# Kernel optimization log

Hardware: AMD Instinct MI355X
Metric: run time of the kernel (lower is better)

Reference implementation:

```python
import jax, jax.numpy as jnp
import numpy as np

B, T, F, H = 32, 8192, 256, 128


def setup_inputs() -> dict:
    key = jax.random.key(0)
    k1, k2, k3, k4, k5 = jax.random.split(key, 5)
    return {
        "encoder_outputs": jax.random.normal(k1, (B, T, F), dtype=jnp.float32),
        "dec_output": jax.random.normal(k2, (B, F), dtype=jnp.float32),
        "W1": jax.random.normal(k3, (F, H), dtype=jnp.float32) * 0.05,
        "W2": jax.random.normal(k4, (F, H), dtype=jnp.float32) * 0.05,
        "V": jax.random.normal(k5, (H, 1), dtype=jnp.float32) * 0.05,
    }


def reference(encoder_outputs, dec_output, W1, W2, V):
    # w1_e: [B,T,H]; w2_d: [B,1,H] (constant across timesteps, no real recurrence)
    w1_e = jnp.einsum("btf,fh->bth", encoder_outputs, W1)
    w2_d = (dec_output @ W2)[:, None, :]
    # scores[b,t] = V . tanh(W1 e_t + W2 d)  -> [B, T] (raw logits, no softmax in original call)
    scores = jnp.einsum("bth,h->bt", jnp.tanh(w1_e + w2_d), V[:, 0])
    return scores
```

## Files before the change

### kernel.cpp

```cpp
#include <hip/hip_runtime.h>

#define B_ 32
#define T_ 8192
#define F_ 256
#define H_ 128

typedef short bf16x8 __attribute__((ext_vector_type(8)));
typedef float f32x4  __attribute__((ext_vector_type(4)));

static __device__ __forceinline__ unsigned int pack_bf2(float lo, float hi) {
    unsigned int r;
    asm("v_cvt_pk_bf16_f32 %0, %1, %2" : "=v"(r) : "v"(lo), "v"(hi));
    return r;
}

static __device__ __forceinline__ float fast_tanh(float x) {
    float e = __builtin_amdgcn_exp2f(x * 2.8853900817779268f);
    return 1.f - 2.f * __builtin_amdgcn_rcpf(e + 1.f);
}

__global__ __launch_bounds__(512) void attn_fused(const float* __restrict__ enc,
                                                  const float* __restrict__ dec,
                                                  const float* __restrict__ W1,
                                                  const float* __restrict__ W2,
                                                  const float* __restrict__ Vvec,
                                                  float* __restrict__ out) {
    __shared__ __align__(16) unsigned char tile_lds[2][32 * 512];
    __shared__ float red[8][512];
    __shared__ float w2dp[4][128];
    __shared__ float w2dv[128];

    const int tid  = threadIdx.x;
    const int blk  = blockIdx.x;
    const int b    = blk >> 4;
    const int t0   = (blk & 15) << 9;
    const int w    = tid >> 6;
    const int lane = tid & 63;
    const int q    = lane >> 4;
    const int c    = lane & 15;

    const f32x4* src = (const f32x4*)(enc + ((size_t)b * T_ + t0) * F_);

    f32x4 x[4];
    #pragma unroll
    for (int i = 0; i < 4; ++i) x[i] = src[i * 512 + tid];

    const int h = 16 * w + c;
    bf16x8 bw[8];
    #pragma unroll
    for (int ks = 0; ks < 8; ++ks) {
        const float* wp = W1 + (64 * q + 8 * ks) * H_ + h;
        union { bf16x8 v; unsigned int u[4]; } pk;
        #pragma unroll
        for (int jj = 0; jj < 4; ++jj)
            pk.u[jj] = pack_bf2(wp[(2 * jj) * H_], wp[(2 * jj + 1) * H_]);
        bw[ks] = pk.v;
    }

    {
        const int hh = tid & 127, p = tid >> 7;
        const float* dp  = dec + b * F_ + p * 64;
        const float* w2p = W2 + (p * 64) * H_ + hh;
        float s = 0.f;
        #pragma unroll 8
        for (int f = 0; f < 64; ++f) s += dp[f] * w2p[f * H_];
        w2dp[p][hh] = s;
    }
    __syncthreads();
    if (tid < 128)
        w2dv[tid] = w2dp[0][tid] + w2dp[1][tid] + w2dp[2][tid] + w2dp[3][tid];
    __syncthreads();

    const float Vv = Vvec[h];
    const float wd = w2dv[h];
    const int sw = c & 7;

    #pragma unroll 2
    for (int ht = 0; ht < 16; ++ht) {
        unsigned char* buf = tile_lds[ht & 1];

        #pragma unroll
        for (int i = 0; i < 4; ++i) {
            const int flat4 = i * 512 + tid;
            const int row   = flat4 >> 6;
            const int c4    = flat4 & 63;
            const int chunk = (c4 >> 1) ^ (row & 7);
            uint2 v;
            v.x = pack_bf2(x[i][0], x[i][1]);
            v.y = pack_bf2(x[i][2], x[i][3]);
            *(uint2*)(buf + row * 512 + chunk * 16 + (c4 & 1) * 8) = v;
        }

        if (ht < 15) {
            const f32x4* sp = src + (ht + 1) * 2048;
            #pragma unroll
            for (int i = 0; i < 4; ++i) x[i] = sp[i * 512 + tid];
        }

        asm volatile("s_waitcnt lgkmcnt(0)\n\ts_barrier" ::: "memory");

        #pragma unroll
        for (int g = 0; g < 2; ++g) {
            const unsigned char* rbase = buf + (g * 16 + c) * 512;
            f32x4 acc = {0.f, 0.f, 0.f, 0.f};
            #pragma unroll
            for (int ks = 0; ks < 8; ++ks) {
                bf16x8 a = *(const bf16x8*)(rbase + ((8 * q + ks) ^ sw) * 16);
                acc = __builtin_amdgcn_mfma_f32_16x16x32_bf16(a, bw[ks], acc, 0, 0, 0);
            }
            f32x4 part;
            #pragma unroll
            for (int r = 0; r < 4; ++r)
                part[r] = Vv * fast_tanh(acc[r] + wd);
            #pragma unroll
            for (int m = 1; m < 16; m <<= 1) {
                #pragma unroll
                for (int r = 0; r < 4; ++r) part[r] += __shfl_xor(part[r], m, 64);
            }
            if (c == 0)
                *(f32x4*)&red[w][ht * 32 + g * 16 + 4 * q] = part;
        }
    }

    __syncthreads();
    float s = 0.f;
    #pragma unroll
    for (int ww = 0; ww < 8; ++ww) s += red[ww][tid];
    out[(size_t)b * T_ + t0 + tid] = s;
}

extern "C" void kernel_launch(void* const* d_in, const int* in_sizes, int n_in,
                              void* d_out, int out_size, void* d_ws, size_t ws_size,
                              hipStream_t stream) {
    const float* enc = (const float*)d_in[0];
    const float* dec = (const float*)d_in[1];
    const float* W1  = (const float*)d_in[2];
    const float* W2  = (const float*)d_in[3];
    const float* V   = (const float*)d_in[4];
    float* out = (float*)d_out;

    attn_fused<<<512, 512, 0, stream>>>(enc, dec, W1, W2, V, out);
}
```

Baseline: 53.85 us.

## Swap MFMA operands so the H dimension lands in rows and shrink blocks to 256 threads

The kernel now uses 256-thread blocks over 256 timesteps, with 1024 blocks in total. Each wave covers 32 hidden units as two 16-wide N tiles and shares one LDS read of the encoder tile between two MFMAs. The MFMA operands are swapped so W1 is the A operand, which puts hidden units across the accumulator rows. The V-weighted tanh sum can then be reduced inside each lane over 8 values, leaving only two cross-lane shuffles instead of sixteen. It also adds s_setprio around the MFMA loop and halves LDS usage per block, which allows more blocks per CU, at the cost of twice the bf16 W1 fragments held in registers.

Result: slower. 58.40 us (+8.5%).

```diff
diff --git a/kernel.cpp b/kernel.cpp
--- a/kernel.cpp
+++ b/kernel.cpp
@@ -19,22 +19,22 @@
     return 1.f - 2.f * __builtin_amdgcn_rcpf(e + 1.f);
 }
 
-__global__ __launch_bounds__(512) void attn_fused(const float* __restrict__ enc,
+__global__ __launch_bounds__(256) void attn_fused(const float* __restrict__ enc,
                                                   const float* __restrict__ dec,
                                                   const float* __restrict__ W1,
                                                   const float* __restrict__ W2,
                                                   const float* __restrict__ Vvec,
                                                   float* __restrict__ out) {
-    __shared__ __align__(16) unsigned char tile_lds[2][32 * 512];
-    __shared__ float red[8][512];
-    __shared__ float w2dp[4][128];
+    __shared__ __align__(16) unsigned char tile_lds[2][16 * 512];
+    __shared__ float red[4][256];
+    __shared__ float w2dp[2][128];
     __shared__ float w2dv[128];
 
     const int tid  = threadIdx.x;
     const int blk  = blockIdx.x;
-    const int b    = blk >> 4;
-    const int t0   = (blk & 15) << 9;
-    const int w    = tid >> 6;
+    const int b    = blk >> 5;
+    const int t0   = (blk & 31) << 8;
+    const int wh   = tid >> 6;
     const int lane = tid & 63;
     const int q    = lane >> 4;
     const int c    = lane & 15;
@@ -43,45 +43,53 @@
 
     f32x4 x[4];
     #pragma unroll
-    for (int i = 0; i < 4; ++i) x[i] = src[i * 512 + tid];
+    for (int i = 0; i < 4; ++i) x[i] = src[i * 256 + tid];
 
-    const int h = 16 * w + c;
-    bf16x8 bw[8];
+    bf16x8 bw[2][8];
     #pragma unroll
-    for (int ks = 0; ks < 8; ++ks) {
-        const float* wp = W1 + (64 * q + 8 * ks) * H_ + h;
-        union { bf16x8 v; unsigned int u[4]; } pk;
+    for (int ntl = 0; ntl < 2; ++ntl) {
+        const int h = 32 * wh + 16 * ntl + c;
         #pragma unroll
-        for (int jj = 0; jj < 4; ++jj)
-            pk.u[jj] = pack_bf2(wp[(2 * jj) * H_], wp[(2 * jj + 1) * H_]);
-        bw[ks] = pk.v;
+        for (int ks = 0; ks < 8; ++ks) {
+            const float* wp = W1 + (64 * q + 8 * ks) * H_ + h;
+            union { bf16x8 v; unsigned int u[4]; } pk;
+            #pragma unroll
+            for (int jj = 0; jj < 4; ++jj)
+                pk.u[jj] = pack_bf2(wp[(2 * jj) * H_], wp[(2 * jj + 1) * H_]);
+            bw[ntl][ks] = pk.v;
+        }
     }
 
     {
         const int hh = tid & 127, p = tid >> 7;
-        const float* dp  = dec + b * F_ + p * 64;
-        const float* w2p = W2 + (p * 64) * H_ + hh;
+        const float* dp  = dec + b * F_ + p * 128;
+        const float* w2p = W2 + (p * 128) * H_ + hh;
         float s = 0.f;
         #pragma unroll 8
-        for (int f = 0; f < 64; ++f) s += dp[f] * w2p[f * H_];
+        for (int f = 0; f < 128; ++f) s += dp[f] * w2p[f * H_];
         w2dp[p][hh] = s;
     }
     __syncthreads();
-    if (tid < 128)
-        w2dv[tid] = w2dp[0][tid] + w2dp[1][tid] + w2dp[2][tid] + w2dp[3][tid];
+    if (tid < 128) w2dv[tid] = w2dp[0][tid] + w2dp[1][tid];
     __syncthreads();
 
-    const float Vv = Vvec[h];
-    const float wd = w2dv[h];
+    float Vv[2][4], wd[2][4];
+    #pragma unroll
+    for (int ntl = 0; ntl < 2; ++ntl)
+        #pragma unroll
+        for (int r = 0; r < 4; ++r) {
+            const int hr = 32 * wh + 16 * ntl + 4 * q + r;
+            Vv[ntl][r] = Vvec[hr];
+            wd[ntl][r] = w2dv[hr];
+        }
     const int sw = c & 7;
 
-    #pragma unroll 2
-    for (int ht = 0; ht < 16; ++ht) {
-        unsigned char* buf = tile_lds[ht & 1];
+    for (int st = 0; st < 16; ++st) {
+        unsigned char* buf = tile_lds[st & 1];
 
         #pragma unroll
         for (int i = 0; i < 4; ++i) {
-            const int flat4 = i * 512 + tid;
+            const int flat4 = i * 256 + tid;
             const int row   = flat4 >> 6;
             const int c4    = flat4 & 63;
             const int chunk = (c4 >> 1) ^ (row & 7);
@@ -91,42 +99,44 @@
             *(uint2*)(buf + row * 512 + chunk * 16 + (c4 & 1) * 8) = v;
         }
 
-        if (ht < 15) {
-            const f32x4* sp = src + (ht + 1) * 2048;
+        if (st < 15) {
+            const f32x4* sp = src + (st + 1) * 1024;
             #pragma unroll
-            for (int i = 0; i < 4; ++i) x[i] = sp[i * 512 + tid];
+            for (int i = 0; i < 4; ++i) x[i] = sp[i * 256 + tid];
         }
 
         asm volatile("s_waitcnt lgkmcnt(0)\n\ts_barrier" ::: "memory");
 
+        __builtin_amdgcn_s_setprio(1);
+        const unsigned char* rbase = buf + c * 512;
+        f32x4 a0 = {0.f, 0.f, 0.f, 0.f};
+        f32x4 a1 = {0.f, 0.f, 0.f, 0.f};
         #pragma unroll
-        for (int g = 0; g < 2; ++g) {
-            const unsigned char* rbase = buf + (g * 16 + c) * 512;
-            f32x4 acc = {0.f, 0.f, 0.f, 0.f};
-            #pragma unroll
-            for (int ks = 0; ks < 8; ++ks) {
-                bf16x8 a = *(const bf16x8*)(rbase + ((8 * q + ks) ^ sw) * 16);
-                acc = __builtin_amdgcn_mfma_f32_16x16x32_bf16(a, bw[ks], acc, 0, 0, 0);
-            }
-            f32x4 part;
-            #pragma unroll
-            for (int r = 0; r < 4; ++r)
-                part[r] = Vv * fast_tanh(acc[r] + wd);
-            #pragma unroll
-            for (int m = 1; m < 16; m <<= 1) {
-                #pragma unroll
-                for (int r = 0; r < 4; ++r) part[r] += __shfl_xor(part[r], m, 64);
-            }
-            if (c == 0)
-                *(f32x4*)&red[w][ht * 32 + g * 16 + 4 * q] = part;
+        for (int ks = 0; ks < 8; ++ks) {
+            bf16x8 be = *(const bf16x8*)(rbase + ((8 * q + ks) ^ sw) * 16);
+            a0 = __builtin_amdgcn_mfma_f32_16x16x32_bf16(bw[0][ks], be, a0, 0, 0, 0);
+            a1 = __builtin_amdgcn_mfma_f32_16x16x32_bf16(bw[1][ks], be, a1, 0, 0, 0);
         }
+        __builtin_amdgcn_s_setprio(0);
+
+        float part = Vv[0][0] * fast_tanh(a0[0] + wd[0][0])
+                   + Vv[0][1] * fast_tanh(a0[1] + wd[0][1])
+                   + Vv[0][2] * fast_tanh(a0[2] + wd[0][2])
+                   + Vv[0][3] * fast_tanh(a0[3] + wd[0][3])
+                   + Vv[1][0] * fast_tanh(a1[0] + wd[1][0])
+                   + Vv[1][1] * fast_tanh(a1[1] + wd[1][1])
+                   + Vv[1][2] * fast_tanh(a1[2] + wd[1][2])
+                   + Vv[1][3] * fast_tanh(a1[3] + wd[1][3]);
+        part += __shfl_xor(part, 16, 64);
+        part += __shfl_xor(part, 32, 64);
+        if (lane < 16) red[wh][st * 16 + c] = part;
     }
 
     __syncthreads();
-    float s = 0.f;
-    #pragma unroll
-    for (int ww = 0; ww < 8; ++ww) s += red[ww][tid];
-    out[(size_t)b * T_ + t0 + tid] = s;
+    {
+        float s = red[0][tid] + red[1][tid] + red[2][tid] + red[3][tid];
+        out[(size_t)b * T_ + t0 + tid] = s;
+    }
 }
 
 extern "C" void kernel_launch(void* const* d_in, const int* in_sizes, int n_in,
@@ -139,5 +149,5 @@
     const float* V   = (const float*)d_in[4];
     float* out = (float*)d_out;
 
-    attn_fused<<<512, 512, 0, stream>>>(enc, dec, W1, W2, V, out);
+    attn_fused<<<1024, 256, 0, stream>>>(enc, dec, W1, W2, V, out);
 }
```

## Transpose MFMA operands so each wave covers 32 hidden units and 16 rows

Applied to the files above, without the earlier changes.

Remaps waves so each handles 32 hidden columns (two 16-wide N tiles) over one 16-row group, with W1 as the A operand and the encoder tile as B. This puts hidden units along accumulator rows, so the V-weighted tanh sum happens mostly within a lane and needs only two cross-lane shuffles instead of sixteen. The W2·d bias is folded in as the initial accumulator. Register use for W1 fragments doubles, the final reduction drops from 8 to 4 partial arrays, and the ht loop unroll pragma is removed.

New measurement: 55.19 us. +2.5%, slower.

```diff
diff --git a/kernel.cpp b/kernel.cpp
--- a/kernel.cpp
+++ b/kernel.cpp
@@ -26,7 +26,7 @@
                                                   const float* __restrict__ Vvec,
                                                   float* __restrict__ out) {
     __shared__ __align__(16) unsigned char tile_lds[2][32 * 512];
-    __shared__ float red[8][512];
+    __shared__ float red[4][512];
     __shared__ float w2dp[4][128];
     __shared__ float w2dv[128];
 
@@ -35,6 +35,8 @@
     const int b    = blk >> 4;
     const int t0   = (blk & 15) << 9;
     const int w    = tid >> 6;
+    const int wh   = w & 3;
+    const int wg   = w >> 2;
     const int lane = tid & 63;
     const int q    = lane >> 4;
     const int c    = lane & 15;
@@ -45,16 +47,19 @@
     #pragma unroll
     for (int i = 0; i < 4; ++i) x[i] = src[i * 512 + tid];
 
-    const int h = 16 * w + c;
-    bf16x8 bw[8];
+    bf16x8 bw[2][8];
     #pragma unroll
-    for (int ks = 0; ks < 8; ++ks) {
-        const float* wp = W1 + (64 * q + 8 * ks) * H_ + h;
-        union { bf16x8 v; unsigned int u[4]; } pk;
+    for (int ntl = 0; ntl < 2; ++ntl) {
+        const int h = 32 * wh + 16 * ntl + c;
         #pragma unroll
-        for (int jj = 0; jj < 4; ++jj)
-            pk.u[jj] = pack_bf2(wp[(2 * jj) * H_], wp[(2 * jj + 1) * H_]);
-        bw[ks] = pk.v;
+        for (int ks = 0; ks < 8; ++ks) {
+            const float* wp = W1 + (64 * q + 8 * ks) * H_ + h;
+            union { bf16x8 v; unsigned int u[4]; } pk;
+            #pragma unroll
+            for (int jj = 0; jj < 4; ++jj)
+                pk.u[jj] = pack_bf2(wp[(2 * jj) * H_], wp[(2 * jj + 1) * H_]);
+            bw[ntl][ks] = pk.v;
+        }
     }
 
     {
@@ -71,11 +76,18 @@
         w2dv[tid] = w2dp[0][tid] + w2dp[1][tid] + w2dp[2][tid] + w2dp[3][tid];
     __syncthreads();
 
-    const float Vv = Vvec[h];
-    const float wd = w2dv[h];
+    f32x4 wd0, wd1;
+    float Vv[2][4];
+    #pragma unroll
+    for (int r = 0; r < 4; ++r) {
+        const int h0 = 32 * wh + 4 * q + r;
+        wd0[r] = w2dv[h0];
+        wd1[r] = w2dv[h0 + 16];
+        Vv[0][r] = Vvec[h0];
+        Vv[1][r] = Vvec[h0 + 16];
+    }
     const int sw = c & 7;
 
-    #pragma unroll 2
     for (int ht = 0; ht < 16; ++ht) {
         unsigned char* buf = tile_lds[ht & 1];
 
@@ -99,34 +111,34 @@
 
         asm volatile("s_waitcnt lgkmcnt(0)\n\ts_barrier" ::: "memory");
 
+        const unsigned char* rbase = buf + (wg * 16 + c) * 512;
+        f32x4 a0 = wd0;
+        f32x4 a1 = wd1;
         #pragma unroll
-        for (int g = 0; g < 2; ++g) {
-            const unsigned char* rbase = buf + (g * 16 + c) * 512;
-            f32x4 acc = {0.f, 0.f, 0.f, 0.f};
-            #pragma unroll
-            for (int ks = 0; ks < 8; ++ks) {
-                bf16x8 a = *(const bf16x8*)(rbase + ((8 * q + ks) ^ sw) * 16);
-                acc = __builtin_amdgcn_mfma_f32_16x16x32_bf16(a, bw[ks], acc, 0, 0, 0);
-            }
-            f32x4 part;
-            #pragma unroll
-            for (int r = 0; r < 4; ++r)
-                part[r] = Vv * fast_tanh(acc[r] + wd);
-            #pragma unroll
-            for (int m = 1; m < 16; m <<= 1) {
-                #pragma unroll
-                for (int r = 0; r < 4; ++r) part[r] += __shfl_xor(part[r], m, 64);
-            }
-            if (c == 0)
-                *(f32x4*)&red[w][ht * 32 + g * 16 + 4 * q] = part;
+        for (int ks = 0; ks < 8; ++ks) {
+            bf16x8 be = *(const bf16x8*)(rbase + ((8 * q + ks) ^ sw) * 16);
+            a0 = __builtin_amdgcn_mfma_f32_16x16x32_bf16(bw[0][ks], be, a0, 0, 0, 0);
+            a1 = __builtin_amdgcn_mfma_f32_16x16x32_bf16(bw[1][ks], be, a1, 0, 0, 0);
         }
+
+        float part = Vv[0][0] * fast_tanh(a0[0])
+                   + Vv[0][1] * fast_tanh(a0[1])
+                   + Vv[0][2] * fast_tanh(a0[2])
+                   + Vv[0][3] * fast_tanh(a0[3])
+                   + Vv[1][0] * fast_tanh(a1[0])
+                   + Vv[1][1] * fast_tanh(a1[1])
+                   + Vv[1][2] * fast_tanh(a1[2])
+                   + Vv[1][3] * fast_tanh(a1[3]);
+        part += __shfl_xor(part, 16, 64);
+        part += __shfl_xor(part, 32, 64);
+        if (lane < 16) red[wh][ht * 32 + wg * 16 + c] = part;
     }
 
     __syncthreads();
-    float s = 0.f;
-    #pragma unroll
-    for (int ww = 0; ww < 8; ++ww) s += red[ww][tid];
-    out[(size_t)b * T_ + t0 + tid] = s;
+    {
+        float s = red[0][tid] + red[1][tid] + red[2][tid] + red[3][tid];
+        out[(size_t)b * T_ + t0 + tid] = s;
+    }
 }
 
 extern "C" void kernel_launch(void* const* d_in, const int* in_sizes, int n_in,
```

## Swap MFMA operands, double tile depth, and pipeline per-tile score reduction

Applied to the files above, without the earlier changes.

The MFMA operands are swapped so each lane's four accumulator values cover four hidden units of one timestep. The V-weighted tanh sum then folds within each lane, and only two cross-lane shuffles are needed instead of sixteen. The tile per iteration grows from 32 to 64 timesteps, with 8 prefetched float4 loads per thread, so there are half as many barrier-separated steps. The final cross-wave reduction moves into the loop behind a double-buffered reduction array. This costs more registers and twice the LDS for the tile, which may lower occupancy.

Result: faster. 52.00 us (-3.4%).

```diff
diff --git a/kernel.cpp b/kernel.cpp
--- a/kernel.cpp
+++ b/kernel.cpp
@@ -25,8 +25,8 @@
                                                   const float* __restrict__ W2,
                                                   const float* __restrict__ Vvec,
                                                   float* __restrict__ out) {
-    __shared__ __align__(16) unsigned char tile_lds[2][32 * 512];
-    __shared__ float red[8][512];
+    __shared__ __align__(16) unsigned char tile_lds[2][64 * 512];
+    __shared__ float red[2][8][64];
     __shared__ float w2dp[4][128];
     __shared__ float w2dv[128];
 
@@ -41,9 +41,9 @@
 
     const f32x4* src = (const f32x4*)(enc + ((size_t)b * T_ + t0) * F_);
 
-    f32x4 x[4];
+    f32x4 x[8];
     #pragma unroll
-    for (int i = 0; i < 4; ++i) x[i] = src[i * 512 + tid];
+    for (int i = 0; i < 8; ++i) x[i] = src[i * 512 + tid];
 
     const int h = 16 * w + c;
     bf16x8 bw[8];
@@ -71,16 +71,20 @@
         w2dv[tid] = w2dp[0][tid] + w2dp[1][tid] + w2dp[2][tid] + w2dp[3][tid];
     __syncthreads();
 
-    const float Vv = Vvec[h];
-    const float wd = w2dv[h];
+    float Vv4[4], wd4[4];
+    #pragma unroll
+    for (int r = 0; r < 4; ++r) {
+        const int hr = 16 * w + 4 * q + r;
+        Vv4[r] = Vvec[hr];
+        wd4[r] = w2dv[hr];
+    }
     const int sw = c & 7;
 
-    #pragma unroll 2
-    for (int ht = 0; ht < 16; ++ht) {
+    for (int ht = 0; ht < 8; ++ht) {
         unsigned char* buf = tile_lds[ht & 1];
 
         #pragma unroll
-        for (int i = 0; i < 4; ++i) {
+        for (int i = 0; i < 8; ++i) {
             const int flat4 = i * 512 + tid;
             const int row   = flat4 >> 6;
             const int c4    = flat4 & 63;
@@ -91,42 +95,48 @@
             *(uint2*)(buf + row * 512 + chunk * 16 + (c4 & 1) * 8) = v;
         }
 
-        if (ht < 15) {
-            const f32x4* sp = src + (ht + 1) * 2048;
+        if (ht < 7) {
+            const f32x4* sp = src + (ht + 1) * 4096;
             #pragma unroll
-            for (int i = 0; i < 4; ++i) x[i] = sp[i * 512 + tid];
+            for (int i = 0; i < 8; ++i) x[i] = sp[i * 512 + tid];
         }
 
         asm volatile("s_waitcnt lgkmcnt(0)\n\ts_barrier" ::: "memory");
 
+        if (ht > 0 && tid < 64) {
+            const int prev = ht - 1;
+            float s = 0.f;
+            #pragma unroll
+            for (int ww = 0; ww < 8; ++ww) s += red[prev & 1][ww][tid];
+            out[(size_t)b * T_ + t0 + prev * 64 + tid] = s;
+        }
+
         #pragma unroll
-        for (int g = 0; g < 2; ++g) {
+        for (int g = 0; g < 4; ++g) {
             const unsigned char* rbase = buf + (g * 16 + c) * 512;
             f32x4 acc = {0.f, 0.f, 0.f, 0.f};
             #pragma unroll
             for (int ks = 0; ks < 8; ++ks) {
-                bf16x8 a = *(const bf16x8*)(rbase + ((8 * q + ks) ^ sw) * 16);
-                acc = __builtin_amdgcn_mfma_f32_16x16x32_bf16(a, bw[ks], acc, 0, 0, 0);
+                bf16x8 be = *(const bf16x8*)(rbase + ((8 * q + ks) ^ sw) * 16);
+                acc = __builtin_amdgcn_mfma_f32_16x16x32_bf16(bw[ks], be, acc, 0, 0, 0);
             }
-            f32x4 part;
-            #pragma unroll
-            for (int r = 0; r < 4; ++r)
-                part[r] = Vv * fast_tanh(acc[r] + wd);
-            #pragma unroll
-            for (int m = 1; m < 16; m <<= 1) {
-                #pragma unroll
-                for (int r = 0; r < 4; ++r) part[r] += __shfl_xor(part[r], m, 64);
-            }
-            if (c == 0)
-                *(f32x4*)&red[w][ht * 32 + g * 16 + 4 * q] = part;
+            float part = Vv4[0] * fast_tanh(acc[0] + wd4[0])
+                       + Vv4[1] * fast_tanh(acc[1] + wd4[1])
+                       + Vv4[2] * fast_tanh(acc[2] + wd4[2])
+                       + Vv4[3] * fast_tanh(acc[3] + wd4[3]);
+            part += __shfl_xor(part, 16, 64);
+            part += __shfl_xor(part, 32, 64);
+            if (lane < 16) red[ht & 1][w][g * 16 + c] = part;
         }
     }
 
-    __syncthreads();
-    float s = 0.f;
-    #pragma unroll
-    for (int ww = 0; ww < 8; ++ww) s += red[ww][tid];
-    out[(size_t)b * T_ + t0 + tid] = s;
+    asm volatile("s_waitcnt lgkmcnt(0)\n\ts_barrier" ::: "memory");
+    if (tid < 64) {
+        float s = 0.f;
+        #pragma unroll
+        for (int ww = 0; ww < 8; ++ww) s += red[1][ww][tid];
+        out[(size_t)b * T_ + t0 + 7 * 64 + tid] = s;
+    }
 }
 
 extern "C" void kernel_launch(void* const* d_in, const int* in_sizes, int n_in,
```
